# Kernel optimization log

Measured on AMD Instinct MI355X. Metric: run time of the kernel, lower is better.

Reference implementation:

```python
import jax, jax.numpy as jnp
import numpy as np

DIM = 768
HEADS = 12


def setup_inputs() -> dict:
    key = jax.random.key(0)
    k1, k2, k3, k4 = jax.random.split(key, 4)
    x = jax.random.normal(k1, (8, 1024, DIM), dtype=jnp.float32)
    # qkv: Linear(dim, 3*dim, bias=False); torch stores weight as (out, in), y = x @ W.T
    w_qkv = jax.random.normal(k2, (3 * DIM, DIM), dtype=jnp.float32) * (DIM ** -0.5)
    w_fc = jax.random.normal(k3, (DIM, DIM), dtype=jnp.float32) * (DIM ** -0.5)
    b_fc = jax.random.normal(k4, (DIM,), dtype=jnp.float32) * 0.02
    return {"x": x, "w_qkv": w_qkv, "w_fc": w_fc, "b_fc": b_fc}


def reference(x, w_qkv, w_fc, b_fc):
    b, n, dim = x.shape
    h = HEADS
    d = dim // h
    qkv = jnp.einsum('bnd,ed->bne', x, w_qkv)  # [b, n, 3*dim]
    q, k, v = jnp.split(qkv, 3, axis=-1)
    # b n (h d) -> b h n d
    q = q.reshape(b, n, h, d).transpose(0, 2, 1, 3)
    k = k.reshape(b, n, h, d).transpose(0, 2, 1, 3)
    v = v.reshape(b, n, h, d).transpose(0, 2, 1, 3)
    # NOTE: original module computes d_k = dim**-0.5 but never applies it.
    scores = jnp.einsum('bhqd,bhkd->bhqk', q, k)  # unscaled, faithful to source
    attn = jax.nn.softmax(scores, axis=-1)
    out = jnp.einsum('bhqk,bhkd->bhqd', attn, v)
    out = out.transpose(0, 2, 1, 3).reshape(b, n, dim)  # b h n d -> b n (h d)
    out = jnp.einsum('bnd,ed->bne', out, w_fc) + b_fc
    return out
```

## Files before the change

kernel.cpp:

```cpp
#include <hip/hip_runtime.h>
#include <cstdint>
#include <cstddef>

typedef __bf16 bf16;
typedef __bf16 bf16x4 __attribute__((ext_vector_type(4)));
typedef __bf16 bf16x8 __attribute__((ext_vector_type(8)));
typedef float f32x4 __attribute__((ext_vector_type(4)));
typedef float f32x16 __attribute__((ext_vector_type(16)));

typedef const __attribute__((address_space(1))) void* gas_ptr;
typedef __attribute__((address_space(3))) void* las_ptr;

#define GLOAD_LDS16(g, l) __builtin_amdgcn_global_load_lds((gas_ptr)(g), (las_ptr)(l), 16, 0, 0)

__global__ void cvt_f32_bf16(const float* __restrict__ in, bf16* __restrict__ out, int n4) {
  int i = blockIdx.x * blockDim.x + threadIdx.x;
  int stride = gridDim.x * blockDim.x;
  for (; i < n4; i += stride) {
    float4 v = reinterpret_cast<const float4*>(in)[i];
    bf16x4 o;
    o[0] = (bf16)v.x; o[1] = (bf16)v.y; o[2] = (bf16)v.z; o[3] = (bf16)v.w;
    reinterpret_cast<bf16x4*>(out)[i] = o;
  }
}

template <int MODE>
__global__ __launch_bounds__(256, 2) void gemm_bt(
    const bf16* __restrict__ A, const bf16* __restrict__ B,
    int M, int N, int K,
    bf16* __restrict__ qb, bf16* __restrict__ kb, bf16* __restrict__ vtb,
    float* __restrict__ out, const float* __restrict__ bias) {
  constexpr int BK = 32;
  __shared__ bf16 ldsA[128 * BK];
  __shared__ bf16 ldsB[128 * BK];
  const int tid = threadIdx.x;
  const int l = tid & 63;
  const int w = tid >> 6;
  const int wr = w >> 1, wc = w & 1;
  const int lr = l & 15, lg = l >> 4;
  const int brow = blockIdx.x * 128;
  const int bcol = blockIdx.y * 128;

  const int srow = tid >> 2;
  const int scol = (tid & 3) * 8;
  const bf16* Ag0 = A + (size_t)(brow + srow) * K + scol;
  const bf16* Ag1 = A + (size_t)(brow + 64 + srow) * K + scol;
  const bf16* Bg0 = B + (size_t)(bcol + srow) * K + scol;
  const bf16* Bg1 = B + (size_t)(bcol + 64 + srow) * K + scol;
  bf16* la0 = &ldsA[tid * 8];
  bf16* la1 = &ldsA[2048 + tid * 8];
  bf16* lb0 = &ldsB[tid * 8];
  bf16* lb1 = &ldsB[2048 + tid * 8];

  f32x4 acc[4][4] = {};

  for (int k0 = 0; k0 < K; k0 += BK) {
    GLOAD_LDS16(Ag0 + k0, la0);
    GLOAD_LDS16(Ag1 + k0, la1);
    GLOAD_LDS16(Bg0 + k0, lb0);
    GLOAD_LDS16(Bg1 + k0, lb1);
    __syncthreads();
    bf16x8 af[4], bfr[4];
#pragma unroll
    for (int mi = 0; mi < 4; mi++)
      af[mi] = *reinterpret_cast<const bf16x8*>(&ldsA[(wr * 64 + mi * 16 + lr) * BK + lg * 8]);
#pragma unroll
    for (int ni = 0; ni < 4; ni++)
      bfr[ni] = *reinterpret_cast<const bf16x8*>(&ldsB[(wc * 64 + ni * 16 + lr) * BK + lg * 8]);
#pragma unroll
    for (int mi = 0; mi < 4; mi++)
#pragma unroll
      for (int ni = 0; ni < 4; ni++)
        acc[mi][ni] = __builtin_amdgcn_mfma_f32_16x16x32_bf16(af[mi], bfr[ni], acc[mi][ni], 0, 0, 0);
    __syncthreads();
  }

#pragma unroll
  for (int mi = 0; mi < 4; mi++) {
#pragma unroll
    for (int r = 0; r < 4; r++) {
      const int m = brow + wr * 64 + mi * 16 + lg * 4 + r;
      const int bb = m >> 10;
      const int npos = m & 1023;
#pragma unroll
      for (int ni = 0; ni < 4; ni++) {
        const int e = bcol + wc * 64 + ni * 16 + lr;
        const float v = acc[mi][ni][r];
        if (MODE == 1) {
          out[(size_t)m * N + e] = v + bias[e];
        } else {
          if (e < 768) {
            const int h = e >> 6, d = e & 63;
            qb[(size_t)(bb * 12 + h) * 65536 + npos * 64 + d] = (bf16)v;
          } else if (e < 1536) {
            const int ee = e - 768;
            const int h = ee >> 6, d = ee & 63;
            kb[(size_t)(bb * 12 + h) * 65536 + npos * 64 + d] = (bf16)v;
          } else {
            const int ee = e - 1536;
            const int h = ee >> 6, d = ee & 63;
            vtb[(size_t)(bb * 12 + h) * 65536 + d * 1024 + npos] = (bf16)v;
          }
        }
      }
    }
  }
}

__global__ __launch_bounds__(256, 3) void attn_kernel(
    const bf16* __restrict__ Q, const bf16* __restrict__ K,
    const bf16* __restrict__ Vt, bf16* __restrict__ Out) {
  __shared__ bf16 Kb[2][4096];
  __shared__ bf16 Vb[2][4096];
  const int tid = threadIdx.x;
  const int l = tid & 63;
  const int w = tid >> 6;
  const int ql = l & 31;
  const int hi = l >> 5;
  const int bh = blockIdx.x;
  const int b = bh / 12, h = bh % 12;
  const int q0 = blockIdx.y * 128 + w * 32;
  const bf16* Qh = Q + (size_t)bh * 65536;
  const bf16* Kh = K + (size_t)bh * 65536;
  const bf16* Vh = Vt + (size_t)bh * 65536;
  constexpr float L2E = 1.4426950408889634f;

  const int kdst0 = (0 * 4 + w) * 512 + l * 8;
  const int kdst1 = (1 * 4 + w) * 512 + l * 8;
  const bf16* ksrc0 = Kh + (0 * 32 + ql) * 64 + w * 16 + hi * 8;
  const bf16* ksrc1 = Kh + (1 * 32 + ql) * 64 + w * 16 + hi * 8;
  const bf16* vsrc0 = Vh + (size_t)((w & 1) * 32 + ql) * 1024 + ((0 * 4 + w) >> 1) * 16 + hi * 8;
  const bf16* vsrc1 = Vh + (size_t)((w & 1) * 32 + ql) * 1024 + ((1 * 4 + w) >> 1) * 16 + hi * 8;

  bf16x8 qf[4];
#pragma unroll
  for (int s = 0; s < 4; s++)
    qf[s] = *reinterpret_cast<const bf16x8*>(&Qh[(size_t)(q0 + ql) * 64 + s * 16 + hi * 8]);

  f32x16 o[2] = {};
  float ls0 = 0.f, ls1 = 0.f, ls2 = 0.f, ls3 = 0.f;

  GLOAD_LDS16(ksrc0, &Kb[0][kdst0]);
  GLOAD_LDS16(ksrc1, &Kb[0][kdst1]);
  GLOAD_LDS16(vsrc0, &Vb[0][kdst0]);
  GLOAD_LDS16(vsrc1, &Vb[0][kdst1]);
  asm volatile("s_waitcnt vmcnt(0)" ::: "memory");
  __syncthreads();

  int p = 0;
  for (int it = 0; it < 16; ++it) {
    const int kt = it * 64;
    if (it < 15) {
      GLOAD_LDS16(ksrc0 + (kt + 64) * 64, &Kb[p ^ 1][kdst0]);
      GLOAD_LDS16(ksrc1 + (kt + 64) * 64, &Kb[p ^ 1][kdst1]);
      GLOAD_LDS16(vsrc0 + (kt + 64), &Vb[p ^ 1][kdst0]);
      GLOAD_LDS16(vsrc1 + (kt + 64), &Vb[p ^ 1][kdst1]);
    }

    bf16x8 kf[8];
#pragma unroll
    for (int r = 0; r < 8; r++)
      kf[r] = *reinterpret_cast<const bf16x8*>(&Kb[p][r * 512 + l * 8]);
    f32x16 st0 = {}, st1 = {};
    __builtin_amdgcn_s_setprio(1);
#pragma unroll
    for (int s = 0; s < 4; s++) {
      st0 = __builtin_amdgcn_mfma_f32_32x32x16_bf16(kf[s], qf[s], st0, 0, 0, 0);
      st1 = __builtin_amdgcn_mfma_f32_32x32x16_bf16(kf[4 + s], qf[s], st1, 0, 0, 0);
    }
    __builtin_amdgcn_s_setprio(0);

#pragma unroll
    for (int r = 0; r < 16; r++) {
      float a0 = st0[r] * L2E, a1 = st1[r] * L2E;
      float e0, e1;
      asm("v_exp_f32 %0, %1" : "=v"(e0) : "v"(a0));
      asm("v_exp_f32 %0, %1" : "=v"(e1) : "v"(a1));
      st0[r] = e0; st1[r] = e1;
    }
#pragma unroll
    for (int r = 0; r < 16; r += 2) {
      ls0 += st0[r]; ls1 += st0[r + 1];
      ls2 += st1[r]; ls3 += st1[r + 1];
    }

    bf16x8 pfv[4];
#pragma unroll
    for (int t = 0; t < 4; t++) {
      const int c8 = (t & 1) * 8;
      const f32x16& sv = (t < 2) ? st0 : st1;
      uint32_t wA0, wA1, wB0, wB1;
      asm("v_cvt_pk_bf16_f32 %0, %1, %2" : "=v"(wA0) : "v"(sv[c8 + 0]), "v"(sv[c8 + 1]));
      asm("v_cvt_pk_bf16_f32 %0, %1, %2" : "=v"(wA1) : "v"(sv[c8 + 2]), "v"(sv[c8 + 3]));
      asm("v_cvt_pk_bf16_f32 %0, %1, %2" : "=v"(wB0) : "v"(sv[c8 + 4]), "v"(sv[c8 + 5]));
      asm("v_cvt_pk_bf16_f32 %0, %1, %2" : "=v"(wB1) : "v"(sv[c8 + 6]), "v"(sv[c8 + 7]));
      asm("v_permlane32_swap_b32 %0, %1" : "+v"(wA0), "+v"(wB0));
      asm("v_permlane32_swap_b32 %0, %1" : "+v"(wA1), "+v"(wB1));
      union { uint32_t u[4]; bf16x8 v; } pf;
      pf.u[0] = wA0; pf.u[1] = wA1; pf.u[2] = wB0; pf.u[3] = wB1;
      pfv[t] = pf.v;
    }

    bf16x8 vf[8];
#pragma unroll
    for (int r = 0; r < 8; r++)
      vf[r] = *reinterpret_cast<const bf16x8*>(&Vb[p][r * 512 + l * 8]);
    __builtin_amdgcn_s_setprio(1);
#pragma unroll
    for (int t = 0; t < 4; t++) {
      o[0] = __builtin_amdgcn_mfma_f32_32x32x16_bf16(vf[t * 2 + 0], pfv[t], o[0], 0, 0, 0);
      o[1] = __builtin_amdgcn_mfma_f32_32x32x16_bf16(vf[t * 2 + 1], pfv[t], o[1], 0, 0, 0);
    }
    __builtin_amdgcn_s_setprio(0);

    asm volatile("s_waitcnt vmcnt(0)" ::: "memory");
    __syncthreads();
    p ^= 1;
  }

  float lsum = (ls0 + ls1) + (ls2 + ls3);
  lsum += __shfl_xor(lsum, 32);
  const float rl = 1.0f / lsum;
  bf16* orow = Out + (size_t)(b * 1024 + q0 + ql) * 768 + h * 64;
#pragma unroll
  for (int dh = 0; dh < 2; dh++)
#pragma unroll
    for (int rq = 0; rq < 4; rq++) {
      union { ushort us[4]; uint2 v; } pk;
#pragma unroll
      for (int i = 0; i < 4; i++) {
        const bf16 hv = (bf16)(o[dh][rq * 4 + i] * rl);
        pk.us[i] = __builtin_bit_cast(ushort, hv);
      }
      *reinterpret_cast<uint2*>(&orow[dh * 32 + rq * 8 + hi * 4]) = pk.v;
    }
}

extern "C" void kernel_launch(void* const* d_in, const int* in_sizes, int n_in,
                              void* d_out, int out_size, void* d_ws, size_t ws_size,
                              hipStream_t stream) {
  const float* x = (const float*)d_in[0];
  const float* w_qkv = (const float*)d_in[1];
  const float* w_fc = (const float*)d_in[2];
  const float* b_fc = (const float*)d_in[3];
  float* out = (float*)d_out;
  char* ws = (char*)d_ws;

  bf16* xb = (bf16*)(ws);
  bf16* wqkb = (bf16*)(ws + 12582912);
  bf16* wfcb = (bf16*)(ws + 16121856);
  bf16* qb = (bf16*)(ws + 17301504);
  bf16* kb = (bf16*)(ws + 29884416);
  bf16* vtb = (bf16*)(ws + 42467328);
  bf16* aob = (bf16*)(ws + 55050240);

  cvt_f32_bf16<<<2048, 256, 0, stream>>>(x, xb, 6291456 / 4);
  cvt_f32_bf16<<<1728, 256, 0, stream>>>(w_qkv, wqkb, 1769472 / 4);
  cvt_f32_bf16<<<576, 256, 0, stream>>>(w_fc, wfcb, 589824 / 4);

  gemm_bt<0><<<dim3(64, 18), 256, 0, stream>>>(xb, wqkb, 8192, 2304, 768,
                                               qb, kb, vtb, nullptr, nullptr);

  attn_kernel<<<dim3(96, 8), 256, 0, stream>>>(qb, kb, vtb, aob);

  gemm_bt<1><<<dim3(64, 6), 256, 0, stream>>>(aob, wfcb, 8192, 768, 768,
                                              nullptr, nullptr, nullptr, out, b_fc);
}
```

Baseline: 136.1 us.

## Double-buffer GEMM loads, swizzle block order, store QKV row-major with separate V transpose

The GEMM now double-buffers its LDS tiles so the global loads for the next K-slice overlap the MFMAs on the current one. It also remaps block IDs so neighbouring workgroups share tiles in cache, and raises the occupancy hint. The QKV projection writes a plain row-major bf16 matrix instead of scattered per-head Q/K and a strided V-transpose, and attention reads Q/K from that layout directly. A new small kernel transposes V through LDS, which adds one launch and an extra pass over V in exchange for coalesced epilogue stores.

```diff
diff --git a/kernel.cpp b/kernel.cpp
--- a/kernel.cpp
+++ b/kernel.cpp
@@ -25,54 +25,65 @@
 }
 
 template <int MODE>
-__global__ __launch_bounds__(256, 2) void gemm_bt(
+__global__ __launch_bounds__(256, 3) void gemm_bt(
     const bf16* __restrict__ A, const bf16* __restrict__ B,
     int M, int N, int K,
-    bf16* __restrict__ qb, bf16* __restrict__ kb, bf16* __restrict__ vtb,
-    float* __restrict__ out, const float* __restrict__ bias) {
+    bf16* __restrict__ outb, float* __restrict__ outf,
+    const float* __restrict__ bias) {
   constexpr int BK = 32;
-  __shared__ bf16 ldsA[128 * BK];
-  __shared__ bf16 ldsB[128 * BK];
+  __shared__ bf16 ldsA[2][4096];
+  __shared__ bf16 ldsB[2][4096];
   const int tid = threadIdx.x;
   const int l = tid & 63;
   const int w = tid >> 6;
   const int wr = w >> 1, wc = w & 1;
   const int lr = l & 15, lg = l >> 4;
-  const int brow = blockIdx.x * 128;
-  const int bcol = blockIdx.y * 128;
-
-  const int srow = tid >> 2;
-  const int scol = (tid & 3) * 8;
-  const bf16* Ag0 = A + (size_t)(brow + srow) * K + scol;
-  const bf16* Ag1 = A + (size_t)(brow + 64 + srow) * K + scol;
-  const bf16* Bg0 = B + (size_t)(bcol + srow) * K + scol;
-  const bf16* Bg1 = B + (size_t)(bcol + 64 + srow) * K + scol;
-  bf16* la0 = &ldsA[tid * 8];
-  bf16* la1 = &ldsA[2048 + tid * 8];
-  bf16* lb0 = &ldsB[tid * 8];
-  bf16* lb1 = &ldsB[2048 + tid * 8];
+
+  const int gx = gridDim.x, nwg = gx * gridDim.y;
+  int bid = blockIdx.y * gx + blockIdx.x;
+  bid = (bid & 7) * (nwg >> 3) + (bid >> 3);
+  const int brow = (bid % gx) * 128;
+  const int bcol = (bid / gx) * 128;
+
+  const bf16* sa0 = A + (size_t)(brow + w * 16 + lr) * K + lg * 8;
+  const bf16* sa1 = sa0 + (size_t)64 * K;
+  const bf16* sb0 = B + (size_t)(bcol + w * 16 + lr) * K + lg * 8;
+  const bf16* sb1 = sb0 + (size_t)64 * K;
+  const int d0 = w * 512 + l * 8;
+  const int d1 = (4 + w) * 512 + l * 8;
 
   f32x4 acc[4][4] = {};
 
+  GLOAD_LDS16(sa0, &ldsA[0][d0]);
+  GLOAD_LDS16(sa1, &ldsA[0][d1]);
+  GLOAD_LDS16(sb0, &ldsB[0][d0]);
+  GLOAD_LDS16(sb1, &ldsB[0][d1]);
+  asm volatile("s_waitcnt vmcnt(0)" ::: "memory");
+  __syncthreads();
+
+  int p = 0;
   for (int k0 = 0; k0 < K; k0 += BK) {
-    GLOAD_LDS16(Ag0 + k0, la0);
-    GLOAD_LDS16(Ag1 + k0, la1);
-    GLOAD_LDS16(Bg0 + k0, lb0);
-    GLOAD_LDS16(Bg1 + k0, lb1);
-    __syncthreads();
+    if (k0 + BK < K) {
+      GLOAD_LDS16(sa0 + (k0 + BK), &ldsA[p ^ 1][d0]);
+      GLOAD_LDS16(sa1 + (k0 + BK), &ldsA[p ^ 1][d1]);
+      GLOAD_LDS16(sb0 + (k0 + BK), &ldsB[p ^ 1][d0]);
+      GLOAD_LDS16(sb1 + (k0 + BK), &ldsB[p ^ 1][d1]);
+    }
     bf16x8 af[4], bfr[4];
 #pragma unroll
     for (int mi = 0; mi < 4; mi++)
-      af[mi] = *reinterpret_cast<const bf16x8*>(&ldsA[(wr * 64 + mi * 16 + lr) * BK + lg * 8]);
+      af[mi] = *reinterpret_cast<const bf16x8*>(&ldsA[p][(wr * 4 + mi) * 512 + l * 8]);
 #pragma unroll
     for (int ni = 0; ni < 4; ni++)
-      bfr[ni] = *reinterpret_cast<const bf16x8*>(&ldsB[(wc * 64 + ni * 16 + lr) * BK + lg * 8]);
+      bfr[ni] = *reinterpret_cast<const bf16x8*>(&ldsB[p][(wc * 4 + ni) * 512 + l * 8]);
 #pragma unroll
     for (int mi = 0; mi < 4; mi++)
 #pragma unroll
       for (int ni = 0; ni < 4; ni++)
         acc[mi][ni] = __builtin_amdgcn_mfma_f32_16x16x32_bf16(af[mi], bfr[ni], acc[mi][ni], 0, 0, 0);
+    asm volatile("s_waitcnt vmcnt(0)" ::: "memory");
     __syncthreads();
+    p ^= 1;
   }
 
 #pragma unroll
@@ -80,36 +91,50 @@
 #pragma unroll
     for (int r = 0; r < 4; r++) {
       const int m = brow + wr * 64 + mi * 16 + lg * 4 + r;
-      const int bb = m >> 10;
-      const int npos = m & 1023;
 #pragma unroll
       for (int ni = 0; ni < 4; ni++) {
         const int e = bcol + wc * 64 + ni * 16 + lr;
         const float v = acc[mi][ni][r];
         if (MODE == 1) {
-          out[(size_t)m * N + e] = v + bias[e];
+          outf[(size_t)m * N + e] = v + bias[e];
         } else {
-          if (e < 768) {
-            const int h = e >> 6, d = e & 63;
-            qb[(size_t)(bb * 12 + h) * 65536 + npos * 64 + d] = (bf16)v;
-          } else if (e < 1536) {
-            const int ee = e - 768;
-            const int h = ee >> 6, d = ee & 63;
-            kb[(size_t)(bb * 12 + h) * 65536 + npos * 64 + d] = (bf16)v;
-          } else {
-            const int ee = e - 1536;
-            const int h = ee >> 6, d = ee & 63;
-            vtb[(size_t)(bb * 12 + h) * 65536 + d * 1024 + npos] = (bf16)v;
-          }
+          outb[(size_t)m * N + e] = (bf16)v;
         }
       }
     }
   }
 }
 
+__global__ __launch_bounds__(256) void vtrans(const bf16* __restrict__ qkv,
+                                              bf16* __restrict__ vtb) {
+  __shared__ bf16 t[64 * 72];
+  const int bh = blockIdx.x;
+  const int b = bh / 12, h = bh % 12;
+  const int nt = blockIdx.y;
+  const int tid = threadIdx.x;
+#pragma unroll
+  for (int it = 0; it < 2; it++) {
+    const int item = tid + it * 256;
+    const int nl = item >> 3, c = item & 7;
+    bf16x8 v = *reinterpret_cast<const bf16x8*>(
+        &qkv[(size_t)(b * 1024 + nt * 64 + nl) * 2304 + 1536 + h * 64 + c * 8]);
+#pragma unroll
+    for (int j = 0; j < 8; j++) t[(c * 8 + j) * 72 + nl] = v[j];
+  }
+  __syncthreads();
+#pragma unroll
+  for (int it = 0; it < 2; it++) {
+    const int item = tid + it * 256;
+    const int d = item >> 3, c2 = item & 7;
+    bf16x8 v = *reinterpret_cast<const bf16x8*>(&t[d * 72 + c2 * 8]);
+    *reinterpret_cast<bf16x8*>(
+        &vtb[(size_t)bh * 65536 + d * 1024 + nt * 64 + c2 * 8]) = v;
+  }
+}
+
 __global__ __launch_bounds__(256, 3) void attn_kernel(
-    const bf16* __restrict__ Q, const bf16* __restrict__ K,
-    const bf16* __restrict__ Vt, bf16* __restrict__ Out) {
+    const bf16* __restrict__ QKV, const bf16* __restrict__ Vt,
+    bf16* __restrict__ Out) {
   __shared__ bf16 Kb[2][4096];
   __shared__ bf16 Vb[2][4096];
   const int tid = threadIdx.x;
@@ -120,22 +145,21 @@
   const int bh = blockIdx.x;
   const int b = bh / 12, h = bh % 12;
   const int q0 = blockIdx.y * 128 + w * 32;
-  const bf16* Qh = Q + (size_t)bh * 65536;
-  const bf16* Kh = K + (size_t)bh * 65536;
   const bf16* Vh = Vt + (size_t)bh * 65536;
   constexpr float L2E = 1.4426950408889634f;
 
   const int kdst0 = (0 * 4 + w) * 512 + l * 8;
   const int kdst1 = (1 * 4 + w) * 512 + l * 8;
-  const bf16* ksrc0 = Kh + (0 * 32 + ql) * 64 + w * 16 + hi * 8;
-  const bf16* ksrc1 = Kh + (1 * 32 + ql) * 64 + w * 16 + hi * 8;
+  const bf16* ksrc0 = QKV + (size_t)(b * 1024 + ql) * 2304 + 768 + h * 64 + w * 16 + hi * 8;
+  const bf16* ksrc1 = ksrc0 + (size_t)32 * 2304;
   const bf16* vsrc0 = Vh + (size_t)((w & 1) * 32 + ql) * 1024 + ((0 * 4 + w) >> 1) * 16 + hi * 8;
   const bf16* vsrc1 = Vh + (size_t)((w & 1) * 32 + ql) * 1024 + ((1 * 4 + w) >> 1) * 16 + hi * 8;
 
+  const bf16* Qrow = QKV + (size_t)(b * 1024 + q0 + ql) * 2304 + h * 64;
   bf16x8 qf[4];
 #pragma unroll
   for (int s = 0; s < 4; s++)
-    qf[s] = *reinterpret_cast<const bf16x8*>(&Qh[(size_t)(q0 + ql) * 64 + s * 16 + hi * 8]);
+    qf[s] = *reinterpret_cast<const bf16x8*>(&Qrow[s * 16 + hi * 8]);
 
   f32x16 o[2] = {};
   float ls0 = 0.f, ls1 = 0.f, ls2 = 0.f, ls3 = 0.f;
@@ -151,8 +175,8 @@
   for (int it = 0; it < 16; ++it) {
     const int kt = it * 64;
     if (it < 15) {
-      GLOAD_LDS16(ksrc0 + (kt + 64) * 64, &Kb[p ^ 1][kdst0]);
-      GLOAD_LDS16(ksrc1 + (kt + 64) * 64, &Kb[p ^ 1][kdst1]);
+      GLOAD_LDS16(ksrc0 + (size_t)(kt + 64) * 2304, &Kb[p ^ 1][kdst0]);
+      GLOAD_LDS16(ksrc1 + (size_t)(kt + 64) * 2304, &Kb[p ^ 1][kdst1]);
       GLOAD_LDS16(vsrc0 + (kt + 64), &Vb[p ^ 1][kdst0]);
       GLOAD_LDS16(vsrc1 + (kt + 64), &Vb[p ^ 1][kdst1]);
     }
@@ -247,11 +271,10 @@
   char* ws = (char*)d_ws;
 
   bf16* xb = (bf16*)(ws);
+  bf16* vtb = (bf16*)(ws);
   bf16* wqkb = (bf16*)(ws + 12582912);
   bf16* wfcb = (bf16*)(ws + 16121856);
-  bf16* qb = (bf16*)(ws + 17301504);
-  bf16* kb = (bf16*)(ws + 29884416);
-  bf16* vtb = (bf16*)(ws + 42467328);
+  bf16* qkvb = (bf16*)(ws + 17301504);
   bf16* aob = (bf16*)(ws + 55050240);
 
   cvt_f32_bf16<<<2048, 256, 0, stream>>>(x, xb, 6291456 / 4);
@@ -259,10 +282,12 @@
   cvt_f32_bf16<<<576, 256, 0, stream>>>(w_fc, wfcb, 589824 / 4);
 
   gemm_bt<0><<<dim3(64, 18), 256, 0, stream>>>(xb, wqkb, 8192, 2304, 768,
-                                               qb, kb, vtb, nullptr, nullptr);
-
-  attn_kernel<<<dim3(96, 8), 256, 0, stream>>>(qb, kb, vtb, aob);
+                                               qkvb, nullptr, nullptr);
+
+  vtrans<<<dim3(96, 16), 256, 0, stream>>>(qkvb, vtb);
+
+  attn_kernel<<<dim3(96, 8), 256, 0, stream>>>(qkvb, vtb, aob);
 
   gemm_bt<1><<<dim3(64, 6), 256, 0, stream>>>(aob, wfcb, 8192, 768, 768,
-                                              nullptr, nullptr, nullptr, out, b_fc);
-}
+                                              nullptr, out, b_fc);
+}
```

Result: slower. 159.5 us (+17.2%).
